# Kernel optimization log

Measured on AMD Instinct MI355X. Metric: run time of the kernel, lower is better.

Reference implementation:

```python
import jax, jax.numpy as jnp
import numpy as np

B, S, E, H, G = 2, 2048, 2048, 16, 4
D = E // H  # head dim = 128


def setup_inputs() -> dict:
    key = jax.random.key(0)
    ks = jax.random.split(key, 7)
    scale = 1.0 / np.sqrt(E)
    x = jax.random.normal(ks[0], (B, S, E), dtype=jnp.float32)
    Wq = jax.random.normal(ks[1], (H, E, D), dtype=jnp.float32) * scale
    bq = jax.random.normal(ks[2], (H, D), dtype=jnp.float32) * 0.02
    Wk = jax.random.normal(ks[3], (G, E, D), dtype=jnp.float32) * scale
    bk = jax.random.normal(ks[4], (G, D), dtype=jnp.float32) * 0.02
    Wv = jax.random.normal(ks[5], (G, E, D), dtype=jnp.float32) * scale
    bv = jax.random.normal(ks[6], (G, D), dtype=jnp.float32) * 0.02
    return {"x": x, "Wq": Wq, "bq": bq, "Wk": Wk, "bk": bk, "Wv": Wv, "bv": bv}


def reference(x, Wq, bq, Wk, bk, Wv, bv):
    # x: [B,S,E]; Wq: [H,E,D]; Wk/Wv: [G,E,D]
    h, e, d = Wq.shape
    g = Wk.shape[0]
    per = h // g  # Q heads per KV group
    s = x.shape[1]

    # batched QKV projections (replaces per-head nn.Linear loop)
    q = jnp.einsum('bse,hed->bhsd', x, Wq) + bq[None, :, None, :]   # [B,H,S,D]
    kg = jnp.einsum('bse,ged->bgsd', x, Wk) + bk[None, :, None, :]  # [B,G,S,D]
    vg = jnp.einsum('bse,ged->bgsd', x, Wv) + bv[None, :, None, :]

    # GQA: each KV group serves `per` consecutive Q heads (order i*per+j)
    k = jnp.repeat(kg, per, axis=1)  # [B,H,S,D]
    v = jnp.repeat(vg, per, axis=1)

    scores = jnp.einsum('bhqd,bhkd->bhqk', q, k) * (1.0 / np.sqrt(d))
    causal = jnp.triu(jnp.ones((s, s), dtype=bool), k=1)  # strict upper = masked
    scores = jnp.where(causal[None, None, :, :], -jnp.inf, scores)
    attn = jax.nn.softmax(scores, axis=-1)
    out = jnp.einsum('bhqk,bhkd->bhqd', attn, v)  # [B,H,S,D]
    # concat per-head outputs along feature dim (head order matches loop order)
    return out.transpose(0, 2, 1, 3).reshape(x.shape[0], s, h * d)
```

## Files before the change

kernel.cpp:

```cpp
#include <hip/hip_runtime.h>
#include <math.h>


typedef __attribute__((ext_vector_type(8))) short bf16x8;
typedef __attribute__((ext_vector_type(4))) short s16x4;
typedef __attribute__((ext_vector_type(4))) float f32x4;

#define LOG2E 1.4426950408889634f

__device__ __forceinline__ short f2bf(float f) {
  union { float f; unsigned u; } v; v.f = f;
  unsigned r = v.u + 0x7FFFu + ((v.u >> 16) & 1u);
  return (short)(r >> 16);
}

__device__ __forceinline__ void async16(const void* g, void* l) {
  __builtin_amdgcn_global_load_lds(
      (const __attribute__((address_space(1))) void*)g,
      (__attribute__((address_space(3))) void*)l, 16, 0, 0);
}

__device__ __forceinline__ f32x4 mfma16(bf16x8 a, bf16x8 b, f32x4 c) {
  return __builtin_amdgcn_mfma_f32_16x16x32_bf16(a, b, c, 0, 0, 0);
}


__global__ void conv_x(const float4* __restrict__ x, s16x4* __restrict__ xb) {
  const int i = blockIdx.x * 256 + threadIdx.x;
  float4 v = x[i];
  s16x4 o;
  o[0] = f2bf(v.x); o[1] = f2bf(v.y); o[2] = f2bf(v.z); o[3] = f2bf(v.w);
  xb[i] = o;
}

__global__ void transpose_w(const float* __restrict__ src, short* __restrict__ wt, int c0) {
  __shared__ float t[32][33];
  const int hh = blockIdx.z;
  const int e0 = blockIdx.x * 32, d0 = blockIdx.y * 32;
  const int tx = threadIdx.x, ty = threadIdx.y;
  const float* s = src + (size_t)hh * 2048 * 128;
#pragma unroll
  for (int i = ty; i < 32; i += 8)
    t[i][tx] = s[(size_t)(e0 + i) * 128 + d0 + tx];
  __syncthreads();
#pragma unroll
  for (int i = ty; i < 32; i += 8)
    wt[(size_t)(c0 + hh * 128 + d0 + i) * 2048 + e0 + tx] = f2bf(t[tx][i]);
}

__global__ void build_bias(const float* __restrict__ bq, const float* __restrict__ bk,
                           const float* __restrict__ bv, float* __restrict__ bc) {
  const int c = blockIdx.x * 256 + threadIdx.x;
  float v;
  if (c < 2048)      v = bq[c];
  else if (c < 2560) v = bk[c - 2048];
  else               v = bv[c - 2560];
  bc[c] = v;
}


__global__ __launch_bounds__(256) void qkv_gemm(
    const short* __restrict__ xb, const short* __restrict__ wt,
    const float* __restrict__ bc,
    short* __restrict__ qb, short* __restrict__ kb, short* __restrict__ vt)
{
  constexpr int E = 2048, BK = 32;
  __shared__ short Al[2][128 * BK];
  __shared__ short Bl[2][128 * BK];
  const int tid = threadIdx.x;
  const int lane = tid & 63, wave = tid >> 6;
  const int wr = wave >> 1, wc = wave & 1;
  const int l16 = lane & 15, grp = lane >> 4;
  const int m0 = blockIdx.y * 128, n0 = blockIdx.x * 128;

  const int c1 = tid, c2 = tid + 256;
  const int r1 = c1 >> 2, s1 = c1 & 3, r2 = c2 >> 2, s2 = c2 & 3;

  f32x4 acc[4][4] = {};

  async16(xb + (size_t)(m0 + r1) * E + s1 * 8, (char*)Al[0] + c1 * 16);
  async16(xb + (size_t)(m0 + r2) * E + s2 * 8, (char*)Al[0] + c2 * 16);
  async16(wt + (size_t)(n0 + r1) * E + s1 * 8, (char*)Bl[0] + c1 * 16);
  async16(wt + (size_t)(n0 + r2) * E + s2 * 8, (char*)Bl[0] + c2 * 16);
  __syncthreads();

  const int nk = E / BK;
  for (int t = 0; t < nk; ++t) {
    const int cur = t & 1;
    if (t + 1 < nk) {
      const int k0 = (t + 1) * BK;
      async16(xb + (size_t)(m0 + r1) * E + k0 + s1 * 8, (char*)Al[cur ^ 1] + c1 * 16);
      async16(xb + (size_t)(m0 + r2) * E + k0 + s2 * 8, (char*)Al[cur ^ 1] + c2 * 16);
      async16(wt + (size_t)(n0 + r1) * E + k0 + s1 * 8, (char*)Bl[cur ^ 1] + c1 * 16);
      async16(wt + (size_t)(n0 + r2) * E + k0 + s2 * 8, (char*)Bl[cur ^ 1] + c2 * 16);
    }
    bf16x8 af[4], bfr[4];
#pragma unroll
    for (int mi = 0; mi < 4; ++mi)
      af[mi] = *(const bf16x8*)&Al[cur][(wr * 64 + mi * 16 + l16) * BK + grp * 8];
#pragma unroll
    for (int ni = 0; ni < 4; ++ni)
      bfr[ni] = *(const bf16x8*)&Bl[cur][(wc * 64 + ni * 16 + l16) * BK + grp * 8];
#pragma unroll
    for (int mi = 0; mi < 4; ++mi)
#pragma unroll
      for (int ni = 0; ni < 4; ++ni)
        acc[mi][ni] = mfma16(af[mi], bfr[ni], acc[mi][ni]);
    __syncthreads();
  }

  const float qscale = 0.08838834764831845f;
#pragma unroll
  for (int ni = 0; ni < 4; ++ni) {
    const int c = n0 + wc * 64 + ni * 16 + l16;
    const float bias = bc[c];
    const int d = c & 127;
#pragma unroll
    for (int mi = 0; mi < 4; ++mi) {
      const int rbase = m0 + wr * 64 + mi * 16 + grp * 4;
      const int b = rbase >> 11;
      const int s = rbase & 2047;
      f32x4 a = acc[mi][ni];
      if (c < 2048) {
        const int h = c >> 7;
        short* dst = qb + ((size_t)(b * 16 + h) * 2048 + s) * 128 + d;
#pragma unroll
        for (int r = 0; r < 4; ++r) dst[(size_t)r * 128] = f2bf((a[r] + bias) * qscale);
      } else if (c < 2560) {
        const int gi = (c >> 7) & 3;
        short* dst = kb + ((size_t)(b * 4 + gi) * 2048 + s) * 128 + d;
#pragma unroll
        for (int r = 0; r < 4; ++r) dst[(size_t)r * 128] = f2bf(a[r] + bias);
      } else {
        const int gi = (c >> 7) & 3;
        s16x4 pk;
#pragma unroll
        for (int r = 0; r < 4; ++r) pk[r] = f2bf(a[r] + bias);
        *(s16x4*)&vt[((size_t)(b * 4 + gi) * 128 + d) * 2048 + s] = pk;
      }
    }
  }
}


__device__ __forceinline__ void stageKV(char* kd, char* vd,
                                        const short* __restrict__ Kg,
                                        const short* __restrict__ Vg,
                                        int kv0, int tid) {
#pragma unroll
  for (int rd = 0; rd < 2; ++rd) {
    const int off = rd * 8192 + tid * 16;
    const int row = off >> 8, colb = off & 255;
    const int sc = colb ^ ((row & 7) << 4);
    async16(Kg + (size_t)(kv0 + row) * 128 + (sc >> 1), kd + off);
  }
#pragma unroll
  for (int rd = 0; rd < 2; ++rd) {
    const int off = rd * 8192 + tid * 16;
    const int row = off >> 7, colb = off & 127;
    const int sc = colb ^ ((row & 7) << 4);
    async16(Vg + (size_t)row * 2048 + kv0 + (sc >> 1), vd + off);
  }
}

__global__ __launch_bounds__(512) void attn(
    const short* __restrict__ qb, const short* __restrict__ kb,
    const short* __restrict__ vt, float* __restrict__ out)
{
  constexpr int S = 2048, D = 128;
  extern __shared__ char lds[];
  char* const Kbuf0 = lds;
  char* const Kbuf1 = lds + 16384;
  char* const Vbuf0 = lds + 32768;
  char* const Vbuf1 = lds + 49152;
  const int tid = threadIdx.x;
  const int lane = tid & 63, wave = tid >> 6;
  const int l16 = lane & 15, grp = lane >> 4;
  const int h = blockIdx.y, b = blockIdx.z;
  const int g = h >> 2;
  const short* Qg = qb + (size_t)(b * 16 + h) * S * D;
  const short* Kg = kb + (size_t)(b * 4 + g) * S * D;
  const short* Vg = vt + (size_t)(b * 4 + g) * (size_t)D * S;
  char* const Pb = lds + 65536 + wave * 2048;
  const int swz = (l16 & 7) << 4;

#pragma unroll
  for (int p = 0; p < 2; ++p) {
    const int jj = p ? (15 - (int)blockIdx.x) : (int)blockIdx.x;
    const int qbase = jj * 128;
    const int q0 = qbase + wave * 16;
    const int kv_end = q0 + 16;

    bf16x8 qf[4];
#pragma unroll
    for (int c = 0; c < 4; ++c)
      qf[c] = *(const bf16x8*)&Qg[(size_t)(q0 + l16) * D + c * 32 + grp * 8];

    f32x4 o[8] = {};
    float mrun = -INFINITY, lrun = 0.f;

    const int nt = (qbase + 128) >> 6;
    stageKV(Kbuf0, Vbuf0, Kg, Vg, 0, tid);
    __syncthreads();

    for (int t = 0; t < nt; ++t) {
      const int kv0 = t << 6;
      char* const Kb = (t & 1) ? Kbuf1 : Kbuf0;
      char* const Vb = (t & 1) ? Vbuf1 : Vbuf0;
      if (t + 1 < nt)
        stageKV((t & 1) ? Kbuf0 : Kbuf1, (t & 1) ? Vbuf0 : Vbuf1, Kg, Vg, kv0 + 64, tid);

      if (kv0 < kv_end) {
        f32x4 st[4] = {};
#pragma unroll
        for (int c = 0; c < 4; ++c)
#pragma unroll
          for (int f = 0; f < 4; ++f) {
            const int row = f * 16 + l16;
            bf16x8 kf = *(const bf16x8*)(Kb + row * 256 + ((c * 64 + grp * 16) ^ swz));
            st[f] = mfma16(kf, qf[c], st[f]);
          }
        if (kv0 + 63 > q0) {
          const int qa = q0 + l16;
#pragma unroll
          for (int f = 0; f < 4; ++f)
#pragma unroll
            for (int r = 0; r < 4; ++r)
              if (kv0 + f * 16 + grp * 4 + r > qa) st[f][r] = -INFINITY;
        }
        float tmax = -INFINITY;
#pragma unroll
        for (int f = 0; f < 4; ++f)
#pragma unroll
          for (int r = 0; r < 4; ++r) tmax = fmaxf(tmax, st[f][r]);
        tmax = fmaxf(tmax, __shfl_xor(tmax, 16));
        tmax = fmaxf(tmax, __shfl_xor(tmax, 32));
        const float mn = fmaxf(mrun, tmax);
        const float fac = exp2f((mrun - mn) * LOG2E);
        float lsum = 0.f;
        float ps[16];
#pragma unroll
        for (int f = 0; f < 4; ++f)
#pragma unroll
          for (int r = 0; r < 4; ++r) {
            const float pv = exp2f((st[f][r] - mn) * LOG2E);
            ps[f * 4 + r] = pv;
            lsum += pv;
          }
        lsum += __shfl_xor(lsum, 16);
        lsum += __shfl_xor(lsum, 32);
        lrun = lrun * fac + lsum;
        mrun = mn;
#pragma unroll
        for (int f8 = 0; f8 < 8; ++f8) o[f8] *= fac;

#pragma unroll
        for (int f = 0; f < 4; ++f) {
          s16x4 pk;
#pragma unroll
          for (int r = 0; r < 4; ++r) pk[r] = f2bf(ps[f * 4 + r]);
          *(s16x4*)(Pb + l16 * 128 + ((f * 32 + grp * 8) ^ swz)) = pk;
        }
        const bf16x8 pb0 = *(const bf16x8*)(Pb + l16 * 128 + ((grp * 16) ^ swz));
        const bf16x8 pb1 = *(const bf16x8*)(Pb + l16 * 128 + ((64 + grp * 16) ^ swz));

#pragma unroll
        for (int f8 = 0; f8 < 8; ++f8) {
          const int row = f8 * 16 + l16;
          bf16x8 vf0 = *(const bf16x8*)(Vb + row * 128 + ((grp * 16) ^ swz));
          o[f8] = mfma16(vf0, pb0, o[f8]);
          bf16x8 vf1 = *(const bf16x8*)(Vb + row * 128 + ((64 + grp * 16) ^ swz));
          o[f8] = mfma16(vf1, pb1, o[f8]);
        }
      }
      __syncthreads();
    }

    const float inv = 1.f / lrun;
    float* orow = out + ((size_t)b * S + q0 + l16) * 2048 + h * D;
#pragma unroll
    for (int f8 = 0; f8 < 8; ++f8) {
      f32x4 v = o[f8] * inv;
      *(f32x4*)&orow[f8 * 16 + grp * 4] = v;
    }
  }
}


extern "C" void kernel_launch(void* const* d_in, const int* in_sizes, int n_in,
                              void* d_out, int out_size, void* d_ws, size_t ws_size,
                              hipStream_t stream) {
  const float* x  = (const float*)d_in[0];
  const float* Wq = (const float*)d_in[1];
  const float* bq = (const float*)d_in[2];
  const float* Wk = (const float*)d_in[3];
  const float* bk = (const float*)d_in[4];
  const float* Wv = (const float*)d_in[5];
  const float* bv = (const float*)d_in[6];
  float* out = (float*)d_out;

  char* ws = (char*)d_ws;
  short* xb = (short*)ws;
  short* wt = (short*)(ws + (size_t)16 * 1024 * 1024);
  float* bc = (float*)(ws + (size_t)28 * 1024 * 1024);
  short* qb = (short*)(ws + (size_t)28 * 1024 * 1024 + 65536);
  short* kb = (short*)((char*)qb + (size_t)16 * 1024 * 1024);
  short* vt = (short*)((char*)kb + (size_t)4 * 1024 * 1024);

  conv_x<<<8192, 256, 0, stream>>>((const float4*)x, (s16x4*)xb);
  dim3 tb(32, 8);
  transpose_w<<<dim3(64, 4, 16), tb, 0, stream>>>(Wq, wt, 0);
  transpose_w<<<dim3(64, 4, 4),  tb, 0, stream>>>(Wk, wt, 2048);
  transpose_w<<<dim3(64, 4, 4),  tb, 0, stream>>>(Wv, wt, 2560);
  build_bias<<<12, 256, 0, stream>>>(bq, bk, bv, bc);
  qkv_gemm<<<dim3(24, 32), 256, 0, stream>>>(xb, wt, bc, qb, kb, vt);

  hipFuncSetAttribute((const void*)attn, hipFuncAttributeMaxDynamicSharedMemorySize, 81920);
  attn<<<dim3(8, 16, 2), 512, 81920, stream>>>(qb, kb, vt, out);
}
```

Before: 261.2 us.

## Retile attention to 64-row blocks, keep P in registers, add lazy rescale and XCD remap

The attention kernel now runs 256-thread blocks over 64-query tiles, with 512 blocks remapped so that blocks sharing a KV group land on the same XCD. The QKV GEMM gets the same XCD-aware block remap. The attention loop drops the LDS round-trip for the P matrix by reading V in a permuted k-order that matches the MFMA accumulator layout, and uses hardware bf16 conversion. It also skips the online-softmax rescale unless the max grows by more than a threshold, and raises wave priority around the MFMA sections. Together these aim to cut LDS traffic, sync overhead and causal tile imbalance, at the cost of more complex indexing and a looser bound on the exponent range.

```diff
diff --git a/kernel.cpp b/kernel.cpp
--- a/kernel.cpp
+++ b/kernel.cpp
@@ -1,10 +1,13 @@
 #include <hip/hip_runtime.h>
+#include <hip/hip_bf16.h>
 #include <math.h>
 
 
 typedef __attribute__((ext_vector_type(8))) short bf16x8;
 typedef __attribute__((ext_vector_type(4))) short s16x4;
 typedef __attribute__((ext_vector_type(4))) float f32x4;
+
+union v8u { bf16x8 v8; s16x4 half[2]; };
 
 #define LOG2E 1.4426950408889634f
 
@@ -12,6 +15,11 @@
   union { float f; unsigned u; } v; v.f = f;
   unsigned r = v.u + 0x7FFFu + ((v.u >> 16) & 1u);
   return (short)(r >> 16);
+}
+
+__device__ __forceinline__ short hwbf(float f) {
+  __hip_bfloat16 h = __float2bfloat16(f);
+  return *(short*)&h;
 }
 
 __device__ __forceinline__ void async16(const void* g, void* l) {
@@ -71,7 +79,8 @@
   const int lane = tid & 63, wave = tid >> 6;
   const int wr = wave >> 1, wc = wave & 1;
   const int l16 = lane & 15, grp = lane >> 4;
-  const int m0 = blockIdx.y * 128, n0 = blockIdx.x * 128;
+  const int work = (blockIdx.x & 7) * 96 + (blockIdx.x >> 3);
+  const int m0 = (work / 24) * 128, n0 = (work % 24) * 128;
 
   const int c1 = tid, c2 = tid + 256;
   const int r1 = c1 >> 2, s1 = c1 & 3, r2 = c2 >> 2, s2 = c2 & 3;
@@ -148,48 +157,46 @@
                                         const short* __restrict__ Vg,
                                         int kv0, int tid) {
 #pragma unroll
-  for (int rd = 0; rd < 2; ++rd) {
-    const int off = rd * 8192 + tid * 16;
+  for (int rd = 0; rd < 4; ++rd) {
+    const int off = rd * 4096 + tid * 16;
     const int row = off >> 8, colb = off & 255;
     const int sc = colb ^ ((row & 7) << 4);
     async16(Kg + (size_t)(kv0 + row) * 128 + (sc >> 1), kd + off);
   }
 #pragma unroll
-  for (int rd = 0; rd < 2; ++rd) {
-    const int off = rd * 8192 + tid * 16;
+  for (int rd = 0; rd < 4; ++rd) {
+    const int off = rd * 4096 + tid * 16;
     const int row = off >> 7, colb = off & 127;
     const int sc = colb ^ ((row & 7) << 4);
     async16(Vg + (size_t)row * 2048 + kv0 + (sc >> 1), vd + off);
   }
 }
 
-__global__ __launch_bounds__(512) void attn(
+__global__ __launch_bounds__(256) void attn(
     const short* __restrict__ qb, const short* __restrict__ kb,
     const short* __restrict__ vt, float* __restrict__ out)
 {
   constexpr int S = 2048, D = 128;
   extern __shared__ char lds[];
-  char* const Kbuf0 = lds;
-  char* const Kbuf1 = lds + 16384;
-  char* const Vbuf0 = lds + 32768;
-  char* const Vbuf1 = lds + 49152;
   const int tid = threadIdx.x;
   const int lane = tid & 63, wave = tid >> 6;
   const int l16 = lane & 15, grp = lane >> 4;
-  const int h = blockIdx.y, b = blockIdx.z;
-  const int g = h >> 2;
+  const int work = (blockIdx.x & 7) * 64 + (blockIdx.x >> 3);
+  const int bg = work >> 6, s6 = work & 63;
+  const int b = bg >> 2, g = bg & 3;
+  const int h = g * 4 + (s6 >> 4);
+  const int x = s6 & 15;
+
   const short* Qg = qb + (size_t)(b * 16 + h) * S * D;
   const short* Kg = kb + (size_t)(b * 4 + g) * S * D;
   const short* Vg = vt + (size_t)(b * 4 + g) * (size_t)D * S;
-  char* const Pb = lds + 65536 + wave * 2048;
   const int swz = (l16 & 7) << 4;
 
 #pragma unroll
   for (int p = 0; p < 2; ++p) {
-    const int jj = p ? (15 - (int)blockIdx.x) : (int)blockIdx.x;
-    const int qbase = jj * 128;
-    const int q0 = qbase + wave * 16;
-    const int kv_end = q0 + 16;
+    const int jj = p ? (31 - x) : x;
+    const int q0 = jj * 64 + wave * 16;
+    const int nt = jj + 1;
 
     bf16x8 qf[4];
 #pragma unroll
@@ -199,80 +206,83 @@
     f32x4 o[8] = {};
     float mrun = -INFINITY, lrun = 0.f;
 
-    const int nt = (qbase + 128) >> 6;
-    stageKV(Kbuf0, Vbuf0, Kg, Vg, 0, tid);
+    stageKV(lds, lds + 32768, Kg, Vg, 0, tid);
     __syncthreads();
 
     for (int t = 0; t < nt; ++t) {
       const int kv0 = t << 6;
-      char* const Kb = (t & 1) ? Kbuf1 : Kbuf0;
-      char* const Vb = (t & 1) ? Vbuf1 : Vbuf0;
+      const int cur = t & 1;
       if (t + 1 < nt)
-        stageKV((t & 1) ? Kbuf0 : Kbuf1, (t & 1) ? Vbuf0 : Vbuf1, Kg, Vg, kv0 + 64, tid);
-
-      if (kv0 < kv_end) {
-        f32x4 st[4] = {};
-#pragma unroll
-        for (int c = 0; c < 4; ++c)
-#pragma unroll
-          for (int f = 0; f < 4; ++f) {
-            const int row = f * 16 + l16;
-            bf16x8 kf = *(const bf16x8*)(Kb + row * 256 + ((c * 64 + grp * 16) ^ swz));
-            st[f] = mfma16(kf, qf[c], st[f]);
-          }
-        if (kv0 + 63 > q0) {
-          const int qa = q0 + l16;
-#pragma unroll
-          for (int f = 0; f < 4; ++f)
-#pragma unroll
-            for (int r = 0; r < 4; ++r)
-              if (kv0 + f * 16 + grp * 4 + r > qa) st[f][r] = -INFINITY;
+        stageKV(lds + (cur ^ 1) * 16384, lds + 32768 + (cur ^ 1) * 16384,
+                Kg, Vg, kv0 + 64, tid);
+      char* const Kb = lds + cur * 16384;
+      char* const Vb = lds + 32768 + cur * 16384;
+
+      f32x4 st[4] = {};
+      __builtin_amdgcn_s_setprio(1);
+#pragma unroll
+      for (int c = 0; c < 4; ++c)
+#pragma unroll
+        for (int f = 0; f < 4; ++f) {
+          const int row = f * 16 + l16;
+          bf16x8 kf = *(const bf16x8*)(Kb + row * 256 + ((c * 64 + grp * 16) ^ swz));
+          st[f] = mfma16(kf, qf[c], st[f]);
         }
-        float tmax = -INFINITY;
+      __builtin_amdgcn_s_setprio(0);
+      if (t == nt - 1) {
+        const int qa = q0 + l16;
 #pragma unroll
         for (int f = 0; f < 4; ++f)
 #pragma unroll
-          for (int r = 0; r < 4; ++r) tmax = fmaxf(tmax, st[f][r]);
-        tmax = fmaxf(tmax, __shfl_xor(tmax, 16));
-        tmax = fmaxf(tmax, __shfl_xor(tmax, 32));
+          for (int r = 0; r < 4; ++r)
+            if (kv0 + f * 16 + grp * 4 + r > qa) st[f][r] = -INFINITY;
+      }
+      float tmax = -INFINITY;
+#pragma unroll
+      for (int f = 0; f < 4; ++f)
+#pragma unroll
+        for (int r = 0; r < 4; ++r) tmax = fmaxf(tmax, st[f][r]);
+      tmax = fmaxf(tmax, __shfl_xor(tmax, 16));
+      tmax = fmaxf(tmax, __shfl_xor(tmax, 32));
+      float fac = 1.0f;
+      if (!__all(tmax <= mrun + 8.0f)) {
         const float mn = fmaxf(mrun, tmax);
-        const float fac = exp2f((mrun - mn) * LOG2E);
-        float lsum = 0.f;
-        float ps[16];
-#pragma unroll
-        for (int f = 0; f < 4; ++f)
-#pragma unroll
-          for (int r = 0; r < 4; ++r) {
-            const float pv = exp2f((st[f][r] - mn) * LOG2E);
-            ps[f * 4 + r] = pv;
-            lsum += pv;
-          }
-        lsum += __shfl_xor(lsum, 16);
-        lsum += __shfl_xor(lsum, 32);
-        lrun = lrun * fac + lsum;
+        fac = exp2f((mrun - mn) * LOG2E);
+#pragma unroll
+        for (int f8 = 0; f8 < 8; ++f8) o[f8] *= fac;
         mrun = mn;
-#pragma unroll
-        for (int f8 = 0; f8 < 8; ++f8) o[f8] *= fac;
-
-#pragma unroll
-        for (int f = 0; f < 4; ++f) {
-          s16x4 pk;
-#pragma unroll
-          for (int r = 0; r < 4; ++r) pk[r] = f2bf(ps[f * 4 + r]);
-          *(s16x4*)(Pb + l16 * 128 + ((f * 32 + grp * 8) ^ swz)) = pk;
+      }
+      float lsum = 0.f;
+      float ps[16];
+#pragma unroll
+      for (int f = 0; f < 4; ++f)
+#pragma unroll
+        for (int r = 0; r < 4; ++r) {
+          const float pv = exp2f((st[f][r] - mrun) * LOG2E);
+          ps[f * 4 + r] = pv;
+          lsum += pv;
         }
-        const bf16x8 pb0 = *(const bf16x8*)(Pb + l16 * 128 + ((grp * 16) ^ swz));
-        const bf16x8 pb1 = *(const bf16x8*)(Pb + l16 * 128 + ((64 + grp * 16) ^ swz));
-
-#pragma unroll
-        for (int f8 = 0; f8 < 8; ++f8) {
-          const int row = f8 * 16 + l16;
-          bf16x8 vf0 = *(const bf16x8*)(Vb + row * 128 + ((grp * 16) ^ swz));
-          o[f8] = mfma16(vf0, pb0, o[f8]);
-          bf16x8 vf1 = *(const bf16x8*)(Vb + row * 128 + ((64 + grp * 16) ^ swz));
-          o[f8] = mfma16(vf1, pb1, o[f8]);
-        }
+      lsum += __shfl_xor(lsum, 16);
+      lsum += __shfl_xor(lsum, 32);
+      lrun = lrun * fac + lsum;
+
+      bf16x8 pba, pbb;
+#pragma unroll
+      for (int i = 0; i < 8; ++i) { pba[i] = hwbf(ps[i]); pbb[i] = hwbf(ps[8 + i]); }
+
+      __builtin_amdgcn_s_setprio(1);
+#pragma unroll
+      for (int f8 = 0; f8 < 8; ++f8) {
+        const char* vrow = Vb + (f8 * 16 + l16) * 128;
+        v8u va, vb2;
+        va.half[0]  = *(const s16x4*)(vrow + ((grp * 8) ^ swz));
+        va.half[1]  = *(const s16x4*)(vrow + ((32 + grp * 8) ^ swz));
+        o[f8] = mfma16(va.v8, pba, o[f8]);
+        vb2.half[0] = *(const s16x4*)(vrow + ((64 + grp * 8) ^ swz));
+        vb2.half[1] = *(const s16x4*)(vrow + ((96 + grp * 8) ^ swz));
+        o[f8] = mfma16(vb2.v8, pbb, o[f8]);
       }
+      __builtin_amdgcn_s_setprio(0);
       __syncthreads();
     }
 
@@ -313,8 +323,8 @@
   transpose_w<<<dim3(64, 4, 4),  tb, 0, stream>>>(Wk, wt, 2048);
   transpose_w<<<dim3(64, 4, 4),  tb, 0, stream>>>(Wv, wt, 2560);
   build_bias<<<12, 256, 0, stream>>>(bq, bk, bv, bc);
-  qkv_gemm<<<dim3(24, 32), 256, 0, stream>>>(xb, wt, bc, qb, kb, vt);
-
-  hipFuncSetAttribute((const void*)attn, hipFuncAttributeMaxDynamicSharedMemorySize, 81920);
-  attn<<<dim3(8, 16, 2), 512, 81920, stream>>>(qb, kb, vt, out);
-}
+  qkv_gemm<<<768, 256, 0, stream>>>(xb, wt, bc, qb, kb, vt);
+
+  (void)hipFuncSetAttribute((const void*)attn, hipFuncAttributeMaxDynamicSharedMemorySize, 65536);
+  attn<<<512, 256, 65536, stream>>>(qb, kb, vt, out);
+}
```

New measurement: 264.5 us. Within noise of the previous version (+1.3%).
